# Kernel tuning notes

Measured on AMD Instinct MI355X. Metric: run time of the kernel, lower is better.

Reference implementation:

```python
import jax, jax.numpy as jnp
import numpy as np

NUM_CODE = 8192
CODE_DIM = 256
BETA = 0.25


def setup_inputs() -> dict:
    key = jax.random.key(0)
    k1, k2 = jax.random.split(key)
    z = jax.random.normal(k1, (16, CODE_DIM, 32, 32), dtype=jnp.float32)
    scale = 1.0 / NUM_CODE
    embedding = jax.random.uniform(k2, (NUM_CODE, CODE_DIM), dtype=jnp.float32,
                                   minval=-scale, maxval=scale)
    return {"z": z, "embedding": embedding}


def reference(z, embedding):
    # z: [b, c, h, w] -> [b, h, w, c]
    b, c, h, w = z.shape
    z_bhwc = jnp.transpose(z, (0, 2, 3, 1))
    z_flat = z_bhwc.reshape(-1, c)  # [N, code_dim]

    # pairwise squared L2 distance: ||z||^2 + ||e||^2 - 2 z e^T  -> [N, num_code]
    dist = (jnp.sum(z_flat ** 2, axis=1, keepdims=True)
            + jnp.sum(embedding ** 2, axis=1)
            - 2.0 * jnp.einsum('nc,dc->nd', z_flat, embedding))
    idx = jnp.argmin(dist, axis=1)  # [N]

    z_quant = embedding[idx].reshape(z_bhwc.shape)  # [b, h, w, c]

    # codebook + commitment loss
    loss = (jnp.mean((jax.lax.stop_gradient(z_quant) - z_bhwc) ** 2)
            + BETA * jnp.mean((z_quant - jax.lax.stop_gradient(z_bhwc)) ** 2))

    # straight-through estimator
    z_st = z_bhwc + jax.lax.stop_gradient(z_quant - z_bhwc)
    z_st = jnp.transpose(z_st, (0, 3, 1, 2))  # [b, c, h, w]

    indices = idx.reshape(b, h * w)
    return z_st, loss, indices
```

## Files before the change

kernel.cpp:

```cpp
#include <hip/hip_runtime.h>

typedef __attribute__((ext_vector_type(4))) int i32x4;
typedef unsigned short u16;
typedef unsigned char u8;
typedef unsigned int u32;
typedef unsigned long long u64;

static constexpr int NROW = 16384;
static constexpr int NCODE = 8192;
static constexpr int ZN = 4194304;
static constexpr int MARGIN_I = 4200;

static constexpr int GCAP = 6;
static constexpr int OCAP = 24;

static constexpr size_t OFF_EB8  = 0;
static constexpr size_t OFF_LOSS = 2097152;
static constexpr size_t OFF_CTR  = 2097156;

__device__ __forceinline__ char q8(float v, float s) {
  int x = __float2int_rn(v * s);
  x = x < -128 ? -128 : (x > 127 ? 127 : x);
  return (char)x;
}

__device__ __forceinline__ int rowmax16(int m) {
  m = max(m, __builtin_amdgcn_update_dpp(m, m, 0x121, 0xf, 0xf, false));
  m = max(m, __builtin_amdgcn_update_dpp(m, m, 0x122, 0xf, 0xf, false));
  m = max(m, __builtin_amdgcn_update_dpp(m, m, 0x124, 0xf, 0xf, false));
  m = max(m, __builtin_amdgcn_update_dpp(m, m, 0x128, 0xf, 0xf, false));
  return m;
}

#pragma clang fp contract(off)
__device__ float np_dist(const float* zr, const float* __restrict__ er, float A) {
  const float4* e4 = (const float4*)er;
  const float4* z4 = (const float4*)zr;
  float s0 = 0.f, s1 = 0.f, s2 = 0.f, s3 = 0.f;
#pragma unroll 4
  for (int i16 = 0; i16 < 16; ++i16) {
    float4 ea = e4[i16 * 4 + 0], eb = e4[i16 * 4 + 1];
    float4 ec = e4[i16 * 4 + 2], ed = e4[i16 * 4 + 3];
    float4 za = z4[i16 * 4 + 0], zb = z4[i16 * 4 + 1];
    float4 zc = z4[i16 * 4 + 2], zd = z4[i16 * 4 + 3];
    s0 = __fadd_rn(__fmul_rn(za.x, ea.x),
         __fadd_rn(__fmul_rn(zb.x, eb.x),
         __fadd_rn(__fmul_rn(zc.x, ec.x),
         __fadd_rn(__fmul_rn(zd.x, ed.x), s0))));
    s1 = __fadd_rn(__fmul_rn(za.y, ea.y),
         __fadd_rn(__fmul_rn(zb.y, eb.y),
         __fadd_rn(__fmul_rn(zc.y, ec.y),
         __fadd_rn(__fmul_rn(zd.y, ed.y), s1))));
    s2 = __fadd_rn(__fmul_rn(za.z, ea.z),
         __fadd_rn(__fmul_rn(zb.z, eb.z),
         __fadd_rn(__fmul_rn(zc.z, ec.z),
         __fadd_rn(__fmul_rn(zd.z, ed.z), s2))));
    s3 = __fadd_rn(__fmul_rn(za.w, ea.w),
         __fadd_rn(__fmul_rn(zb.w, eb.w),
         __fadd_rn(__fmul_rn(zc.w, ec.w),
         __fadd_rn(__fmul_rn(zd.w, ed.w), s3))));
  }
  float C = __fadd_rn(__fadd_rn(s0, s1), __fadd_rn(s2, s3));
  return __fadd_rn(A, -(2.0f * C));
}

__device__ float np_rowA(const float* zrow, int lane, volatile float* red) {
  if (lane < 16) {
    const int half = lane >> 3, jj = lane & 7;
    const float* p = zrow + half * 128 + jj;
    float acc = __fmul_rn(p[0], p[0]);
    for (int i = 8; i < 128; i += 8) acc = __fadd_rn(acc, __fmul_rn(p[i], p[i]));
    red[lane] = acc;
  }
  float h0 = __fadd_rn(__fadd_rn(__fadd_rn(red[0], red[1]), __fadd_rn(red[2], red[3])),
                       __fadd_rn(__fadd_rn(red[4], red[5]), __fadd_rn(red[6], red[7])));
  float h1 = __fadd_rn(__fadd_rn(__fadd_rn(red[8], red[9]), __fadd_rn(red[10], red[11])),
                       __fadd_rn(__fadd_rn(red[12], red[13]), __fadd_rn(red[14], red[15])));
  return __fadd_rn(h0, h1);
}
#pragma clang fp contract(fast)

__global__ __launch_bounds__(256) void eprep_kernel(const float* __restrict__ e,
                                                    char* __restrict__ eb8,
                                                    float* __restrict__ loss_ws,
                                                    int* __restrict__ ctr) {
  const int G = blockIdx.x * 256 + threadIdx.x;
  if (G == 0) { *loss_ws = 0.f; *ctr = 0; }
  const int tile = G >> 8, r = G & 255;
  const int kb = r >> 6, lane = r & 63;
  const int l4 = lane >> 4, l15 = lane & 15;
  const float* s = e + (size_t)(tile * 16 + l15) * 256 + kb * 64 + l4 * 16;
  union { char c[16]; i32x4 v; } u;
#pragma unroll
  for (int j = 0; j < 16; ++j) u.c[j] = q8(s[j], 1048576.0f);
  *(i32x4*)(eb8 + (size_t)G * 16) = u.v;
}

__global__ __launch_bounds__(512, 2) void fused_kernel(const float* __restrict__ z,
                                                       const char* __restrict__ eb8,
                                                       const float* __restrict__ emb,
                                                       float* __restrict__ loss_ws,
                                                       int* __restrict__ ctr,
                                                       float* __restrict__ z_st,
                                                       float* __restrict__ out_loss,
                                                       float* __restrict__ out_idx) {
  __shared__ float zrows[32][260];
  __shared__ int s_rm[32];
  __shared__ u32 s_cnt[32][16];
  __shared__ u32 s_ovf[32];
  __shared__ u16 s_slots[32][120];
  __shared__ float red_s[8][16];
  __shared__ float A_s[32], D_s[32];
  __shared__ u64 best_s[32];
  __shared__ int widx_s[32], starts[33], ovf_list[32], rowtot[32];
  __shared__ int nP, nOvf;
  __shared__ u8 cnts8[32][17];
  __shared__ u16 grpoff[32][17];
  __shared__ u16 pidx[32 * 120];

  const int bh = blockIdx.x;
  const int b = bh >> 5, h = bh & 31;
  const int n0 = bh * 32;
  const int tid = threadIdx.x;
  const int wave = tid >> 6, lane = tid & 63;
  const int l15 = lane & 15, l4 = lane >> 4;

  {
    const float* src = z + (size_t)b * 262144 + h * 32;
    const int w = tid & 31, c16 = tid >> 5;
#pragma unroll
    for (int c0 = 0; c0 < 256; c0 += 16) {
      int c = c0 + c16;
      zrows[w][c] = src[(size_t)c * 1024 + w];
    }
  }
  if (tid < 32) { s_rm[tid] = INT_MIN; s_ovf[tid] = 0; best_s[tid] = ~0ull; }
  s_cnt[tid >> 4][tid & 15] = 0;
  __syncthreads();

  i32x4 a[2][4];
#pragma unroll
  for (int rt = 0; rt < 2; ++rt) {
    const float* zr = zrows[rt * 16 + l15];
#pragma unroll
    for (int kb = 0; kb < 4; ++kb) {
      const float4* z4 = (const float4*)(zr + kb * 64 + l4 * 16);
      float4 f0 = z4[0], f1 = z4[1], f2 = z4[2], f3 = z4[3];
      union { char c[16]; i32x4 v; } u;
      u.c[0]  = q8(f0.x, 16.0f); u.c[1]  = q8(f0.y, 16.0f);
      u.c[2]  = q8(f0.z, 16.0f); u.c[3]  = q8(f0.w, 16.0f);
      u.c[4]  = q8(f1.x, 16.0f); u.c[5]  = q8(f1.y, 16.0f);
      u.c[6]  = q8(f1.z, 16.0f); u.c[7]  = q8(f1.w, 16.0f);
      u.c[8]  = q8(f2.x, 16.0f); u.c[9]  = q8(f2.y, 16.0f);
      u.c[10] = q8(f2.z, 16.0f); u.c[11] = q8(f2.w, 16.0f);
      u.c[12] = q8(f3.x, 16.0f); u.c[13] = q8(f3.y, 16.0f);
      u.c[14] = q8(f3.z, 16.0f); u.c[15] = q8(f3.w, 16.0f);
      a[rt][kb] = u.v;
    }
  }

  const i32x4* ebase = (const i32x4*)eb8;
  int lmax[2][4];

#define LOADB(CH, B0, B1, B2, B3)                                                \
  {                                                                              \
    const i32x4* bt = ebase + (size_t)((CH) * 8 + wave) * 256;                   \
    B0 = bt[lane]; B1 = bt[64 + lane]; B2 = bt[128 + lane]; B3 = bt[192 + lane]; \
  }

#define MFMA8(B0, B1, B2, B3, ACC)                                               \
  _Pragma("unroll")                                                              \
  for (int rt = 0; rt < 2; ++rt) {                                               \
    ACC[rt] = __builtin_amdgcn_mfma_i32_16x16x64_i8(a[rt][0], B0, ACC[rt], 0, 0, 0); \
    ACC[rt] = __builtin_amdgcn_mfma_i32_16x16x64_i8(a[rt][1], B1, ACC[rt], 0, 0, 0); \
    ACC[rt] = __builtin_amdgcn_mfma_i32_16x16x64_i8(a[rt][2], B2, ACC[rt], 0, 0, 0); \
    ACC[rt] = __builtin_amdgcn_mfma_i32_16x16x64_i8(a[rt][3], B3, ACC[rt], 0, 0, 0); \
  }

#define SYNC_THR()                                                               \
  {                                                                              \
    _Pragma("unroll")                                                            \
    for (int rt = 0; rt < 2; ++rt)                                               \
      _Pragma("unroll")                                                          \
      for (int r = 0; r < 4; ++r) {                                              \
        int m = rowmax16(lmax[rt][r]);                                           \
        if (l15 == 0) atomicMax(&s_rm[rt * 16 + l4 * 4 + r], m);                 \
      }                                                                          \
    asm volatile("s_waitcnt lgkmcnt(0)\n\ts_barrier" ::: "memory");              \
    _Pragma("unroll")                                                            \
    for (int rt = 0; rt < 2; ++rt)                                               \
      _Pragma("unroll")                                                          \
      for (int r = 0; r < 4; ++r)                                                \
        lmax[rt][r] = max(lmax[rt][r], s_rm[rt * 16 + l4 * 4 + r]);              \
  }

  {
    i32x4 b0, b1, b2, b3;
#pragma unroll 1
    for (int ch = 0; ch < 2; ++ch) {
      LOADB(ch, b0, b1, b2, b3);
      i32x4 acc[2] = {{0,0,0,0},{0,0,0,0}};
      MFMA8(b0, b1, b2, b3, acc);
      if (ch == 0) {
#pragma unroll
        for (int rt = 0; rt < 2; ++rt)
#pragma unroll
          for (int r = 0; r < 4; ++r) lmax[rt][r] = acc[rt][r];
      } else {
#pragma unroll
        for (int rt = 0; rt < 2; ++rt)
#pragma unroll
          for (int r = 0; r < 4; ++r) lmax[rt][r] = max(lmax[rt][r], acc[rt][r]);
      }
    }
  }
  SYNC_THR();

  {
    i32x4 c0_, c1_, c2_, c3_, n0_, n1_, n2_, n3_, t0_, t1_, t2_, t3_;
    LOADB(0, c0_, c1_, c2_, c3_);
    LOADB(1, n0_, n1_, n2_, n3_);
#pragma unroll 1
    for (int ch = 0; ch < 64; ++ch) {
      if (ch < 62) LOADB(ch + 2, t0_, t1_, t2_, t3_);
      i32x4 acc[2] = {{0,0,0,0},{0,0,0,0}};
      MFMA8(c0_, c1_, c2_, c3_, acc);
      const int grp = (ch >> 5) * 8 + wave;
#pragma unroll
      for (int rt = 0; rt < 2; ++rt)
#pragma unroll
        for (int r = 0; r < 4; ++r) {
          const int v = acc[rt][r];
          const bool p = v > lmax[rt][r] - MARGIN_I;
          if (__any(p)) {
            if (p) {
              const int rl = rt * 16 + l4 * 4 + r;
              u32 q = atomicAdd(&s_cnt[rl][grp], 1u);
              if (q < GCAP) {
                s_slots[rl][grp * GCAP + q] = (u16)(ch * 128 + wave * 16 + l15);
              } else {
                u32 o = atomicAdd(&s_ovf[rl], 1u);
                if (o < OCAP)
                  s_slots[rl][96 + o] = (u16)(ch * 128 + wave * 16 + l15);
              }
            }
          }
          lmax[rt][r] = max(lmax[rt][r], v);
        }
      if ((ch & 3) == 3 && ch != 63) SYNC_THR();
      c0_ = n0_; c1_ = n1_; c2_ = n2_; c3_ = n3_;
      n0_ = t0_; n1_ = t1_; n2_ = t2_; n3_ = t3_;
    }
  }
#undef LOADB
#undef MFMA8
#undef SYNC_THR
  __syncthreads();

  for (int j = 0; j < 4; ++j) {
    const int r = wave * 4 + j;
    float A = np_rowA(zrows[r], lane, red_s[wave]);
    if (lane == 0) A_s[r] = A;
  }
  if (tid < 32) {
    const int r = tid;
    int tot = 0;
#pragma unroll
    for (int k = 0; k < 16; ++k) {
      int c = (int)s_cnt[r][k];
      int cc = c > GCAP ? GCAP : c;
      cnts8[r][k] = (u8)cc;
      grpoff[r][k] = (u16)tot;
      tot += cc;
    }
    const int ov = (int)s_ovf[r];
    const int oc = ov > OCAP ? OCAP : ov;
    cnts8[r][16] = (u8)oc;
    grpoff[r][16] = (u16)tot;
    tot += oc;
    rowtot[r] = (ov > OCAP) ? 0 : tot;
  }
  __syncthreads();
  if (tid == 0) {
    int acc = 0, no = 0;
    for (int r = 0; r < 32; ++r) {
      starts[r] = acc;
      acc += rowtot[r];
      if (rowtot[r] == 0) ovf_list[no++] = r;
    }
    starts[32] = acc; nP = acc; nOvf = no;
  }
  __syncthreads();
  {
    const int r = tid >> 4, g = tid & 15;
    if (rowtot[r]) {
      const int c = cnts8[r][g];
      const int base = starts[r] + grpoff[r][g];
      const int sb = g * GCAP;
      for (int j = 0; j < c; ++j) pidx[base + j] = s_slots[r][sb + j];
    }
  }
  if (tid < 32) {
    const int r = tid;
    if (rowtot[r]) {
      const int c = cnts8[r][16];
      const int base = starts[r] + grpoff[r][16];
      for (int j = 0; j < c; ++j) pidx[base + j] = s_slots[r][96 + j];
    }
  }
  __syncthreads();

  const int P = nP;
  for (int p = tid; p < P; p += 512) {
    int lo = 0, hi = 32;
#pragma unroll
    for (int s = 0; s < 5; ++s) {
      int mid = (lo + hi) >> 1;
      if (starts[mid] <= p) lo = mid; else hi = mid;
    }
    const int r = lo, idx = (int)pidx[p];
    float D = np_dist(zrows[r], emb + (size_t)idx * 256, A_s[r]);
    u64 key = ((u64)__float_as_uint(D) << 16) | (u32)idx;
    atomicMin(&best_s[r], key);
  }
  __syncthreads();

  for (int i = 0; i < nOvf; ++i) {
    const int r = ovf_list[i];
    for (int idx = tid; idx < NCODE; idx += 512) {
      float D = np_dist(zrows[r], emb + (size_t)idx * 256, A_s[r]);
      u64 k = ((u64)__float_as_uint(D) << 16) | (u32)idx;
      atomicMin(&best_s[r], k);
    }
  }
  if (nOvf) __syncthreads();

  if (tid < 32) {
    const int r = tid;
    const u64 k = best_s[r];
    const int bidx = (int)(k & 0xFFFF);
    widx_s[r] = bidx;
    out_idx[n0 + r] = (float)bidx;
    D_s[r] = __uint_as_float((u32)(k >> 16));
  }
  __syncthreads();
  if (tid == 0) {
    float s = 0.f;
    for (int r = 0; r < 32; ++r) s += D_s[r];
    atomicAdd(loss_ws, s);
    __threadfence();
    int t = atomicAdd(ctr, 1);
    if (t == 511)
      *out_loss = atomicAdd(loss_ws, 0.0f) * (1.25f / 4194304.0f);
  }

  {
    const int col = tid & 255, hi = tid >> 8;
#pragma unroll
    for (int wi0 = 0; wi0 < 16; ++wi0) {
      const int wi = wi0 * 2 + hi;
      zrows[wi][col] = emb[(size_t)widx_s[wi] * 256 + col];
    }
  }
  __syncthreads();
  {
    const int w = tid & 31, c0 = (tid >> 5) & 7, hi = tid >> 8;
    float* dst = z_st + (size_t)b * 262144 + h * 32 + w;
#pragma unroll
    for (int cj = 0; cj < 16; ++cj) {
      int c = c0 + (cj * 2 + hi) * 8;
      dst[(size_t)c * 1024] = zrows[w][c];
    }
  }
}

extern "C" void kernel_launch(void* const* d_in, const int* in_sizes, int n_in,
                              void* d_out, int out_size, void* d_ws, size_t ws_size,
                              hipStream_t stream) {
  const float* z = (const float*)d_in[0];
  const float* emb = (const float*)d_in[1];
  char* ws = (char*)d_ws;
  char* eb8 = ws + OFF_EB8;
  float* loss_ws = (float*)(ws + OFF_LOSS);
  int* ctr = (int*)(ws + OFF_CTR);
  float* out = (float*)d_out;
  float* out_loss = out + ZN;
  float* out_idx = out + ZN + 1;

  eprep_kernel<<<512, 256, 0, stream>>>(emb, eb8, loss_ws, ctr);
  fused_kernel<<<512, 512, 0, stream>>>(z, eb8, emb, loss_ws, ctr,
                                        out, out_loss, out_idx);
}
```

Measured before the change: 184.4 us.

## Hand-schedule codebook loads with inline asm and explicit vmcnt double buffering

Codebook chunk loads in the main scan loop now use inline global_load_dwordx4 asm with explicit s_waitcnt vmcnt and sched_barrier. The loop is unrolled by two with ping-pong register buffers, replacing the compiler-scheduled triple-buffered prefetch. The candidate threshold (shared row max minus margin) is also precomputed at each sync, which takes a subtraction out of every compare. The aim is tighter control over memory/MFMA overlap and lower VGPR pressure. The costs are a shorter prefetch distance, a looser threshold between syncs that can admit more candidates, and the risk that the compiler touches asm outputs before their wait.

```diff
diff --git a/kernel.cpp b/kernel.cpp
--- a/kernel.cpp
+++ b/kernel.cpp
@@ -160,12 +160,22 @@
   }
 
   const i32x4* ebase = (const i32x4*)eb8;
-  int lmax[2][4];
-
-#define LOADB(CH, B0, B1, B2, B3)                                                \
+  int lmax[2][4], thr[2][4];
+
+#define LOADB_C(CH, B0, B1, B2, B3)                                              \
   {                                                                              \
     const i32x4* bt = ebase + (size_t)((CH) * 8 + wave) * 256;                   \
     B0 = bt[lane]; B1 = bt[64 + lane]; B2 = bt[128 + lane]; B3 = bt[192 + lane]; \
+  }
+
+#define LOADB_ASM(CH, B0, B1, B2, B3)                                            \
+  {                                                                              \
+    const char* bt_ = (const char*)(ebase + (size_t)((CH) * 8 + wave) * 256)     \
+                      + (size_t)lane * 16;                                       \
+    asm volatile("global_load_dwordx4 %0, %1, off"             : "=v"(B0) : "v"(bt_)); \
+    asm volatile("global_load_dwordx4 %0, %1, off offset:1024" : "=v"(B1) : "v"(bt_)); \
+    asm volatile("global_load_dwordx4 %0, %1, off offset:2048" : "=v"(B2) : "v"(bt_)); \
+    asm volatile("global_load_dwordx4 %0, %1, off offset:3072" : "=v"(B3) : "v"(bt_)); \
   }
 
 #define MFMA8(B0, B1, B2, B3, ACC)                                               \
@@ -176,6 +186,29 @@
     ACC[rt] = __builtin_amdgcn_mfma_i32_16x16x64_i8(a[rt][2], B2, ACC[rt], 0, 0, 0); \
     ACC[rt] = __builtin_amdgcn_mfma_i32_16x16x64_i8(a[rt][3], B3, ACC[rt], 0, 0, 0); \
   }
+
+#define CHECK8(CH, ACC)                                                          \
+  _Pragma("unroll")                                                              \
+  for (int rt = 0; rt < 2; ++rt)                                                 \
+    _Pragma("unroll")                                                            \
+    for (int r = 0; r < 4; ++r) {                                                \
+      const int v = ACC[rt][r];                                                  \
+      const bool p = v > thr[rt][r];                                             \
+      if (__any(p)) {                                                            \
+        if (p) {                                                                 \
+          const int rl = rt * 16 + l4 * 4 + r;                                   \
+          u32 q = atomicAdd(&s_cnt[rl][grp_], 1u);                               \
+          if (q < GCAP) {                                                        \
+            s_slots[rl][grp_ * GCAP + q] = (u16)((CH) * 128 + wave * 16 + l15);  \
+          } else {                                                               \
+            u32 o = atomicAdd(&s_ovf[rl], 1u);                                   \
+            if (o < OCAP)                                                        \
+              s_slots[rl][96 + o] = (u16)((CH) * 128 + wave * 16 + l15);         \
+          }                                                                      \
+        }                                                                        \
+      }                                                                          \
+      lmax[rt][r] = max(lmax[rt][r], v);                                         \
+    }
 
 #define SYNC_THR()                                                               \
   {                                                                              \
@@ -191,14 +224,14 @@
     for (int rt = 0; rt < 2; ++rt)                                               \
       _Pragma("unroll")                                                          \
       for (int r = 0; r < 4; ++r)                                                \
-        lmax[rt][r] = max(lmax[rt][r], s_rm[rt * 16 + l4 * 4 + r]);              \
+        thr[rt][r] = s_rm[rt * 16 + l4 * 4 + r] - MARGIN_I;                      \
   }
 
   {
     i32x4 b0, b1, b2, b3;
 #pragma unroll 1
     for (int ch = 0; ch < 2; ++ch) {
-      LOADB(ch, b0, b1, b2, b3);
+      LOADB_C(ch, b0, b1, b2, b3);
       i32x4 acc[2] = {{0,0,0,0},{0,0,0,0}};
       MFMA8(b0, b1, b2, b3, acc);
       if (ch == 0) {
@@ -217,43 +250,40 @@
   SYNC_THR();
 
   {
-    i32x4 c0_, c1_, c2_, c3_, n0_, n1_, n2_, n3_, t0_, t1_, t2_, t3_;
-    LOADB(0, c0_, c1_, c2_, c3_);
-    LOADB(1, n0_, n1_, n2_, n3_);
+    i32x4 c0_, c1_, c2_, c3_, n0_, n1_, n2_, n3_;
+    LOADB_ASM(0, c0_, c1_, c2_, c3_);
 #pragma unroll 1
-    for (int ch = 0; ch < 64; ++ch) {
-      if (ch < 62) LOADB(ch + 2, t0_, t1_, t2_, t3_);
-      i32x4 acc[2] = {{0,0,0,0},{0,0,0,0}};
-      MFMA8(c0_, c1_, c2_, c3_, acc);
-      const int grp = (ch >> 5) * 8 + wave;
-#pragma unroll
-      for (int rt = 0; rt < 2; ++rt)
-#pragma unroll
-        for (int r = 0; r < 4; ++r) {
-          const int v = acc[rt][r];
-          const bool p = v > lmax[rt][r] - MARGIN_I;
-          if (__any(p)) {
-            if (p) {
-              const int rl = rt * 16 + l4 * 4 + r;
-              u32 q = atomicAdd(&s_cnt[rl][grp], 1u);
-              if (q < GCAP) {
-                s_slots[rl][grp * GCAP + q] = (u16)(ch * 128 + wave * 16 + l15);
-              } else {
-                u32 o = atomicAdd(&s_ovf[rl], 1u);
-                if (o < OCAP)
-                  s_slots[rl][96 + o] = (u16)(ch * 128 + wave * 16 + l15);
-              }
-            }
-          }
-          lmax[rt][r] = max(lmax[rt][r], v);
-        }
-      if ((ch & 3) == 3 && ch != 63) SYNC_THR();
-      c0_ = n0_; c1_ = n1_; c2_ = n2_; c3_ = n3_;
-      n0_ = t0_; n1_ = t1_; n2_ = t2_; n3_ = t3_;
-    }
-  }
-#undef LOADB
+    for (int ch = 0; ch < 64; ch += 2) {
+      LOADB_ASM(ch + 1, n0_, n1_, n2_, n3_);
+      asm volatile("s_waitcnt vmcnt(4)" ::: "memory");
+      __builtin_amdgcn_sched_barrier(0);
+      {
+        i32x4 acc[2] = {{0,0,0,0},{0,0,0,0}};
+        MFMA8(c0_, c1_, c2_, c3_, acc);
+        const int grp_ = (ch >> 5) * 8 + wave;
+        CHECK8(ch, acc);
+      }
+      if (ch + 2 < 64) {
+        LOADB_ASM(ch + 2, c0_, c1_, c2_, c3_);
+        asm volatile("s_waitcnt vmcnt(4)" ::: "memory");
+      } else {
+        asm volatile("s_waitcnt vmcnt(0)" ::: "memory");
+      }
+      __builtin_amdgcn_sched_barrier(0);
+      {
+        i32x4 acc[2] = {{0,0,0,0},{0,0,0,0}};
+        MFMA8(n0_, n1_, n2_, n3_, acc);
+        const int grp_ = ((ch + 1) >> 5) * 8 + wave;
+        CHECK8(ch + 1, acc);
+      }
+      if (((ch + 1) & 3) == 3 && (ch + 1) != 63) SYNC_THR();
+    }
+    asm volatile("s_waitcnt vmcnt(0)" ::: "memory");
+  }
+#undef LOADB_C
+#undef LOADB_ASM
 #undef MFMA8
+#undef CHECK8
 #undef SYNC_THR
   __syncthreads();
 
```

Result: faster. 173.4 us (-6.0%).
